# Kernel tuning notes

Measured on AMD Instinct MI355X. Metric: run time of the kernel, lower is better.

Reference implementation:

```python
import jax, jax.numpy as jnp
import numpy as np

D_MODEL = 2048
N_HEADS = 16
D_HEAD = D_MODEL // N_HEADS
EPS = 1e-5


def _layernorm(x, g, b):
    m = jnp.mean(x, axis=-1, keepdims=True)
    v = jnp.mean(jnp.square(x - m), axis=-1, keepdims=True)
    return (x - m) * jax.lax.rsqrt(v + EPS) * g + b


def _mha(x, Wq, bq, Wk, bk, Wv, bv, Wo, bo):
    b, s, _ = x.shape
    # torch Linear: y = x @ W.T + b ; W is [out, in]
    q = (x @ Wq.T + bq).reshape(b, s, N_HEADS, D_HEAD).transpose(0, 2, 1, 3)
    k = (x @ Wk.T + bk).reshape(b, s, N_HEADS, D_HEAD).transpose(0, 2, 1, 3)
    v = (x @ Wv.T + bv).reshape(b, s, N_HEADS, D_HEAD).transpose(0, 2, 1, 3)
    scores = jnp.einsum('bhqd,bhkd->bhqk', q, k) / np.sqrt(D_HEAD).astype(np.float32)
    score = jax.nn.softmax(scores, axis=-1)
    o = jnp.einsum('bhqk,bhkd->bhqd', score, v)
    # NOTE: original does .contiguous().view(b, -1, d_model) WITHOUT transposing
    # heads back -> head-major flattening. Replicated faithfully via reshape.
    o = o.reshape(b, s, D_MODEL)
    return o @ Wo.T + bo, score


def setup_inputs() -> dict:
    key = jax.random.key(0)
    ks = jax.random.split(key, 16)
    sd = 1.0 / np.sqrt(D_MODEL)
    sdf = 1.0 / np.sqrt(4 * D_MODEL)
    d = {
        'x': jax.random.normal(ks[0], (2, 2048, D_MODEL), jnp.float32),
        'Wq': jax.random.uniform(ks[1], (D_MODEL, D_MODEL), jnp.float32, -sd, sd),
        'bq': jnp.zeros((D_MODEL,), jnp.float32),
        'Wk': jax.random.uniform(ks[2], (D_MODEL, D_MODEL), jnp.float32, -sd, sd),
        'bk': jnp.zeros((D_MODEL,), jnp.float32),
        'Wv': jax.random.uniform(ks[3], (D_MODEL, D_MODEL), jnp.float32, -sd, sd),
        'bv': jnp.zeros((D_MODEL,), jnp.float32),
        'Wo': jax.random.uniform(ks[4], (D_MODEL, D_MODEL), jnp.float32, -sd, sd),
        'bo': jnp.zeros((D_MODEL,), jnp.float32),
        'ln1_g': jnp.ones((D_MODEL,), jnp.float32),
        'ln1_b': jnp.zeros((D_MODEL,), jnp.float32),
        'W1': jax.random.uniform(ks[5], (4 * D_MODEL, D_MODEL), jnp.float32, -sd, sd),
        'b1': jnp.zeros((4 * D_MODEL,), jnp.float32),
        'W2': jax.random.uniform(ks[6], (D_MODEL, 4 * D_MODEL), jnp.float32, -sdf, sdf),
        'b2': jnp.zeros((D_MODEL,), jnp.float32),
        'ln2_g': jnp.ones((D_MODEL,), jnp.float32),
        'ln2_b': jnp.zeros((D_MODEL,), jnp.float32),
    }
    return d


def reference(x, Wq, bq, Wk, bk, Wv, bv, Wo, bo, ln1_g, ln1_b, W1, b1, W2, b2, ln2_g, ln2_b):
    # Pre-norm self-attention block (is_post_norm=False, is_cross=False).
    # Dropout is identity (eval mode).
    x_ = _layernorm(x, ln1_g, ln1_b)
    attn_out, score = _mha(x_, Wq, bq, Wk, bk, Wv, bv, Wo, bo)
    x = x + attn_out
    x_ = _layernorm(x, ln2_g, ln2_b)
    h = jax.nn.relu(x_ @ W1.T + b1)
    x = x + (h @ W2.T + b2)
    return x, score
```

## Files before the change

### kernel.cpp

```cpp
#include <hip/hip_runtime.h>
#include <math.h>

#define D_MODEL 2048
#define NHEADS  16
#define DHEAD   128
#define SEQ     2048
#define BATCH   2
#define ROWS    (BATCH * SEQ)
#define D_FF    (4 * D_MODEL)

typedef __attribute__((ext_vector_type(8))) short bf16x8;
typedef __attribute__((ext_vector_type(4))) float f32x4;

__device__ __forceinline__ unsigned short f2bf(float f) {
    unsigned int u = __float_as_uint(f);
    u += 0x7fffu + ((u >> 16) & 1u);
    return (unsigned short)(u >> 16);
}

__device__ __forceinline__ float block_reduce(float v, int is_max) {
    __shared__ float tmp[4];
    #pragma unroll
    for (int o = 32; o > 0; o >>= 1) {
        float other = __shfl_down(v, o, 64);
        v = is_max ? fmaxf(v, other) : (v + other);
    }
    __syncthreads();
    if ((threadIdx.x & 63) == 0) tmp[threadIdx.x >> 6] = v;
    __syncthreads();
    float r = is_max ? fmaxf(fmaxf(tmp[0], tmp[1]), fmaxf(tmp[2], tmp[3]))
                     : (tmp[0] + tmp[1] + tmp[2] + tmp[3]);
    return r;
}

__global__ __launch_bounds__(256)
void castbf_kernel(const float* __restrict__ in, unsigned short* __restrict__ out, int n4)
{
    int i = blockIdx.x * 256 + threadIdx.x;
    if (i < n4) {
        float4 v = ((const float4*)in)[i];
        ushort4 o;
        o.x = f2bf(v.x); o.y = f2bf(v.y); o.z = f2bf(v.z); o.w = f2bf(v.w);
        ((ushort4*)out)[i] = o;
    }
}

__global__ __launch_bounds__(256)
void ln_kernel(const float* __restrict__ x, const float* __restrict__ g,
               const float* __restrict__ b, unsigned short* __restrict__ y)
{
    __shared__ float row[D_MODEL];
    const long r = blockIdx.x;
    const float4* xr = (const float4*)(x + r * D_MODEL);
    float s = 0.f;
    for (int i = threadIdx.x; i < D_MODEL / 4; i += 256) {
        float4 v = xr[i];
        ((float4*)row)[i] = v;
        s += v.x + v.y + v.z + v.w;
    }
    s = block_reduce(s, 0);
    const float mean = s * (1.f / D_MODEL);
    float vs = 0.f;
    for (int i = threadIdx.x; i < D_MODEL / 4; i += 256) {
        float4 v = ((const float4*)row)[i];
        float dx = v.x - mean; vs += dx * dx;
        dx = v.y - mean; vs += dx * dx;
        dx = v.z - mean; vs += dx * dx;
        dx = v.w - mean; vs += dx * dx;
    }
    vs = block_reduce(vs, 0);
    const float inv = rsqrtf(vs * (1.f / D_MODEL) + 1e-5f);
    const float4* g4 = (const float4*)g;
    const float4* b4 = (const float4*)b;
    for (int i = threadIdx.x; i < D_MODEL / 4; i += 256) {
        float4 v = ((const float4*)row)[i];
        float4 gg = g4[i], bb = b4[i];
        ushort4 o;
        o.x = f2bf((v.x - mean) * inv * gg.x + bb.x);
        o.y = f2bf((v.y - mean) * inv * gg.y + bb.y);
        o.z = f2bf((v.z - mean) * inv * gg.z + bb.z);
        o.w = f2bf((v.w - mean) * inv * gg.w + bb.w);
        *(ushort4*)(y + r * D_MODEL + i * 4) = o;
    }
}

__global__ __launch_bounds__(256)
void softmax_kernel(float* __restrict__ sc)
{
    __shared__ float row[SEQ];
    float* p = sc + (long)blockIdx.x * SEQ;
    float m = -1e30f;
    for (int i = threadIdx.x; i < SEQ / 4; i += 256) {
        float4 v = ((const float4*)p)[i];
        ((float4*)row)[i] = v;
        m = fmaxf(m, fmaxf(fmaxf(v.x, v.y), fmaxf(v.z, v.w)));
    }
    m = block_reduce(m, 1);
    float sum = 0.f;
    for (int i = threadIdx.x; i < SEQ; i += 256) {
        float e = expf(row[i] - m);
        row[i] = e;
        sum += e;
    }
    sum = block_reduce(sum, 0);
    const float inv = 1.f / sum;
    for (int i = threadIdx.x; i < SEQ / 4; i += 256) {
        float4 v = ((const float4*)p)[i];
        v.x = row[i * 4 + 0] * inv; v.y = row[i * 4 + 1] * inv;
        v.z = row[i * 4 + 2] * inv; v.w = row[i * 4 + 3] * inv;
        ((float4*)p)[i] = v;
    }
}

constexpr int BK = 64;

__device__ __forceinline__ void stage_tile_f32(const float* g, int ld,
                                               unsigned short* lds, int t)
{
    const int row = t >> 1;
    const int half = t & 1;
    char* lbase = (char*)lds + row * 128;
    const float* gr = g + (size_t)row * ld + half * 32;
    #pragma unroll
    for (int c4 = 0; c4 < 4; ++c4) {
        float4 f0 = *(const float4*)(gr + c4 * 8);
        float4 f1 = *(const float4*)(gr + c4 * 8 + 4);
        bf16x8 v;
        v[0] = (short)f2bf(f0.x); v[1] = (short)f2bf(f0.y);
        v[2] = (short)f2bf(f0.z); v[3] = (short)f2bf(f0.w);
        v[4] = (short)f2bf(f1.x); v[5] = (short)f2bf(f1.y);
        v[6] = (short)f2bf(f1.z); v[7] = (short)f2bf(f1.w);
        const int cs = (half * 4 + c4) ^ (row & 7);
        *(bf16x8*)(lbase + cs * 16) = v;
    }
}

__device__ __forceinline__ void stage_tile_bf(const unsigned short* g, int ld,
                                              unsigned short* lds, int t)
{
    const int row = t >> 1;
    const int half = t & 1;
    char* lbase = (char*)lds + row * 128;
    const unsigned short* gr = g + (size_t)row * ld + half * 32;
    #pragma unroll
    for (int c4 = 0; c4 < 4; ++c4) {
        bf16x8 v = *(const bf16x8*)(gr + c4 * 8);
        const int cs = (half * 4 + c4) ^ (row & 7);
        *(bf16x8*)(lbase + cs * 16) = v;
    }
}

__device__ __forceinline__ void stage_lds(const unsigned short* gbase, int ld,
                                          unsigned short* lds, int wid, int lane)
{
    const int l8 = lane >> 3, c8 = lane & 7;
    #pragma unroll
    for (int i = 0; i < 4; ++i) {
        const int rowb = wid * 32 + i * 8;
        const unsigned short* src = gbase + (size_t)(rowb + l8) * ld + c8 * 8;
        unsigned short* dst = lds + rowb * 64;
        __builtin_amdgcn_global_load_lds(
            (const __attribute__((address_space(1))) unsigned int*)src,
            (__attribute__((address_space(3))) unsigned int*)dst, 16, 0, 0);
    }
}

template<bool AF32, bool OUTBF>
__global__ __launch_bounds__(256)
void gemm_mfma(const void* __restrict__ Av, int lda,
               const unsigned short* __restrict__ B, int ldb,
               const float* __restrict__ bias, int biasM,
               const float* __restrict__ resid,
               void* __restrict__ Cv, int ldc,
               int Kdim, float scale, int relu,
               long sAb, long sAh, long sBb, long sBh, long sCb, long sCh,
               int nh)
{
    __shared__ unsigned short As[128 * BK];
    __shared__ unsigned short Bs[128 * BK];

    const int z  = blockIdx.z;
    const int zb = z / nh, zh = z % nh;
    const long aoff = zb * sAb + zh * sAh;
    const float*          Af = (const float*)Av + (AF32 ? aoff : 0);
    const unsigned short* Ah = (const unsigned short*)Av + (AF32 ? 0 : aoff);
    B += zb * sBb + zh * sBh;
    const long coff = zb * sCb + zh * sCh;
    float*          Cf = (float*)Cv + coff;
    unsigned short* Ch = (unsigned short*)Cv + coff;

    const int bm = blockIdx.y * 128;
    const int bn = blockIdx.x * 128;
    const int t  = threadIdx.x;
    const int lane = t & 63;
    const int wid  = t >> 6;
    const int wr = wid >> 1, wc = wid & 1;
    const int li = lane & 15;
    const int g  = lane >> 4;

    f32x4 acc[4][4];
    #pragma unroll
    for (int i = 0; i < 4; ++i)
        #pragma unroll
        for (int j = 0; j < 4; ++j) acc[i][j] = (f32x4){0.f, 0.f, 0.f, 0.f};

    int aoffs[4], boffs[4];
    #pragma unroll
    for (int m = 0; m < 4; ++m) {
        const int ra = wr * 64 + m * 16 + li;
        const int rb = wc * 64 + m * 16 + li;
        if (AF32) {
            aoffs[m] = ra * 128 + ((g ^ (ra & 7)) << 4);
            boffs[m] = rb * 128 + ((g ^ (rb & 7)) << 4);
        } else {
            aoffs[m] = ra * 128 + (g << 4);
            boffs[m] = rb * 128 + (g << 4);
        }
    }

    for (int k0 = 0; k0 < Kdim; k0 += BK) {
        if (AF32) {
            stage_tile_f32(Af + (size_t)bm * lda + k0, lda, As, t);
            stage_tile_bf (B  + (size_t)bn * ldb + k0, ldb, Bs, t);
        } else {
            stage_lds(Ah + (size_t)bm * lda + k0, lda, As, wid, lane);
            stage_lds(B  + (size_t)bn * ldb + k0, ldb, Bs, wid, lane);
        }
        __syncthreads();
        #pragma unroll
        for (int kk = 0; kk < 2; ++kk) {
            const int kb = kk * 64;
            bf16x8 a[4], b[4];
            #pragma unroll
            for (int m = 0; m < 4; ++m) {
                a[m] = *(const bf16x8*)((const char*)As + (aoffs[m] ^ kb));
                b[m] = *(const bf16x8*)((const char*)Bs + (boffs[m] ^ kb));
            }
            #pragma unroll
            for (int m = 0; m < 4; ++m)
                #pragma unroll
                for (int n = 0; n < 4; ++n)
                    acc[m][n] = __builtin_amdgcn_mfma_f32_16x16x32_bf16(
                                    a[m], b[n], acc[m][n], 0, 0, 0);
        }
        __syncthreads();
    }

    const int g4 = g * 4;
    #pragma unroll
    for (int m = 0; m < 4; ++m) {
        #pragma unroll
        for (int n = 0; n < 4; ++n) {
            const int c = bn + wc * 64 + n * 16 + li;
            #pragma unroll
            for (int r = 0; r < 4; ++r) {
                const long R = bm + wr * 64 + m * 16 + g4 + r;
                float v = acc[m][n][r] * scale;
                if (bias)  v += biasM ? bias[R] : bias[c];
                if (resid) v += resid[R * (long)ldc + c];
                if (relu)  v = fmaxf(v, 0.f);
                if (OUTBF) Ch[R * (long)ldc + c] = f2bf(v);
                else       Cf[R * (long)ldc + c] = v;
            }
        }
    }
}

extern "C" void kernel_launch(void* const* d_in, const int* in_sizes, int n_in,
                              void* d_out, int out_size, void* d_ws, size_t ws_size,
                              hipStream_t stream)
{
    const float* x    = (const float*)d_in[0];
    const float* Wq   = (const float*)d_in[1];
    const float* bq   = (const float*)d_in[2];
    const float* Wk   = (const float*)d_in[3];
    const float* bk   = (const float*)d_in[4];
    const float* Wv   = (const float*)d_in[5];
    const float* bv   = (const float*)d_in[6];
    const float* Wo   = (const float*)d_in[7];
    const float* bo   = (const float*)d_in[8];
    const float* ln1g = (const float*)d_in[9];
    const float* ln1b = (const float*)d_in[10];
    const float* W1   = (const float*)d_in[11];
    const float* b1   = (const float*)d_in[12];
    const float* W2   = (const float*)d_in[13];
    const float* b2   = (const float*)d_in[14];
    const float* ln2g = (const float*)d_in[15];
    const float* ln2b = (const float*)d_in[16];

    const long XN = (long)ROWS * D_MODEL;
    float* out_x     = (float*)d_out;
    float* out_score = out_x + XN;

    char* w = (char*)d_ws;
    unsigned short* Qb   = (unsigned short*)(w);
    unsigned short* Kb   = (unsigned short*)(w + (16u << 20));
    unsigned short* Vtb  = (unsigned short*)(w + (32u << 20));
    unsigned short* xlnb = (unsigned short*)(w + (48u << 20));
    unsigned short* hb   = (unsigned short*)(w + (64u << 20));
    float*          x1   = (float*)         (w + (128u << 20));
    unsigned short* Wqb  = (unsigned short*)(w + (160u << 20));
    unsigned short* Wkb  = (unsigned short*)(w + (168u << 20));
    unsigned short* Wvb  = (unsigned short*)(w + (176u << 20));
    unsigned short* Wob  = (unsigned short*)(w + (184u << 20));
    unsigned short* W1b  = (unsigned short*)(w + (192u << 20));
    unsigned short* W2b  = (unsigned short*)(w + (224u << 20));
    unsigned short* Ohb   = xlnb;
    unsigned short* xln2b = Kb;

    const dim3 blk(256);
    const float one = 1.f;
    const float qk_scale = 0.08838834764831843f;
    const long Z4M = (long)SEQ * D_MODEL;
    const long ZSC = (long)SEQ * SEQ;
    const long ZOH = (long)SEQ * DHEAD;

    const int nW = D_MODEL * D_MODEL / 4, nF = D_FF * D_MODEL / 4;
    hipLaunchKernelGGL(castbf_kernel, dim3(nW / 256), blk, 0, stream, Wq, Wqb, nW);
    hipLaunchKernelGGL(castbf_kernel, dim3(nW / 256), blk, 0, stream, Wk, Wkb, nW);
    hipLaunchKernelGGL(castbf_kernel, dim3(nW / 256), blk, 0, stream, Wv, Wvb, nW);
    hipLaunchKernelGGL(castbf_kernel, dim3(nW / 256), blk, 0, stream, Wo, Wob, nW);
    hipLaunchKernelGGL(castbf_kernel, dim3(nF / 256), blk, 0, stream, W1, W1b, nF);
    hipLaunchKernelGGL(castbf_kernel, dim3(nF / 256), blk, 0, stream, W2, W2b, nF);

    hipLaunchKernelGGL(ln_kernel, dim3(ROWS), blk, 0, stream, x, ln1g, ln1b, xlnb);

    hipLaunchKernelGGL((gemm_mfma<false, true>), dim3(D_MODEL / 128, ROWS / 128, 1), blk, 0, stream,
                       xlnb, D_MODEL, Wqb, D_MODEL, bq, 0, nullptr, Qb, D_MODEL,
                       D_MODEL, one, 0, 0L, 0L, 0L, 0L, 0L, 0L, 1);
    hipLaunchKernelGGL((gemm_mfma<false, true>), dim3(D_MODEL / 128, ROWS / 128, 1), blk, 0, stream,
                       xlnb, D_MODEL, Wkb, D_MODEL, bk, 0, nullptr, Kb, D_MODEL,
                       D_MODEL, one, 0, 0L, 0L, 0L, 0L, 0L, 0L, 1);
    hipLaunchKernelGGL((gemm_mfma<false, true>), dim3(SEQ / 128, D_MODEL / 128, BATCH), blk, 0, stream,
                       Wvb, D_MODEL, xlnb, D_MODEL, bv, 1, nullptr, Vtb, SEQ,
                       D_MODEL, one, 0, 0L, 0L, Z4M, 0L, Z4M, 0L, 1);

    hipLaunchKernelGGL((gemm_mfma<false, false>), dim3(SEQ / 128, SEQ / 128, BATCH * NHEADS), blk, 0, stream,
                       Qb, D_MODEL, Kb, D_MODEL, nullptr, 0, nullptr, out_score, SEQ,
                       DHEAD, qk_scale, 0,
                       Z4M, (long)DHEAD, Z4M, (long)DHEAD, (long)NHEADS * ZSC, ZSC, NHEADS);

    hipLaunchKernelGGL(softmax_kernel, dim3(BATCH * NHEADS * SEQ), blk, 0, stream, out_score);

    hipLaunchKernelGGL((gemm_mfma<true, true>), dim3(DHEAD / 128, SEQ / 128, BATCH * NHEADS), blk, 0, stream,
                       out_score, SEQ, Vtb, SEQ, nullptr, 0, nullptr, Ohb, DHEAD,
                       SEQ, one, 0,
                       (long)NHEADS * ZSC, ZSC, Z4M, (long)DHEAD * SEQ,
                       (long)NHEADS * ZOH, ZOH, NHEADS);

    hipLaunchKernelGGL((gemm_mfma<false, false>), dim3(D_MODEL / 128, ROWS / 128, 1), blk, 0, stream,
                       Ohb, D_MODEL, Wob, D_MODEL, bo, 0, x, x1, D_MODEL,
                       D_MODEL, one, 0, 0L, 0L, 0L, 0L, 0L, 0L, 1);

    hipLaunchKernelGGL(ln_kernel, dim3(ROWS), blk, 0, stream, x1, ln2g, ln2b, xln2b);

    hipLaunchKernelGGL((gemm_mfma<false, true>), dim3(D_FF / 128, ROWS / 128, 1), blk, 0, stream,
                       xln2b, D_MODEL, W1b, D_MODEL, b1, 0, nullptr, hb, D_FF,
                       D_MODEL, one, 1, 0L, 0L, 0L, 0L, 0L, 0L, 1);

    hipLaunchKernelGGL((gemm_mfma<false, false>), dim3(D_MODEL / 128, ROWS / 128, 1), blk, 0, stream,
                       hb, D_FF, W2b, D_FF, b2, 0, x1, out_x, D_MODEL,
                       D_FF, one, 0, 0L, 0L, 0L, 0L, 0L, 0L, 1);
}
```

Before: 2.006 ms.

## Emit bf16 probabilities from softmax and stage GEMM epilogue through LDS

Softmax now also writes a bf16 copy of the probabilities, and it reads the normalized values from LDS instead of re-reading global memory. This lets the PV GEMM take bf16 input through the async global_load_lds path, replacing the fp32 staging path with per-element conversion. Every GEMM epilogue now goes through a swizzled LDS buffer so each thread stores contiguous 32-column row segments with vector stores, replacing scattered scalar stores. The cost is an extra bf16 write of the whole score tensor and extra syncs and LDS traffic in the epilogue.

```diff
diff --git a/kernel.cpp b/kernel.cpp
--- a/kernel.cpp
+++ b/kernel.cpp
@@ -85,10 +85,11 @@
 }
 
 __global__ __launch_bounds__(256)
-void softmax_kernel(float* __restrict__ sc)
+void softmax_kernel(float* __restrict__ sc, unsigned short* __restrict__ pb)
 {
     __shared__ float row[SEQ];
     float* p = sc + (long)blockIdx.x * SEQ;
+    unsigned short* pbf = pb + (long)blockIdx.x * SEQ;
     float m = -1e30f;
     for (int i = threadIdx.x; i < SEQ / 4; i += 256) {
         float4 v = ((const float4*)p)[i];
@@ -105,50 +106,16 @@
     sum = block_reduce(sum, 0);
     const float inv = 1.f / sum;
     for (int i = threadIdx.x; i < SEQ / 4; i += 256) {
-        float4 v = ((const float4*)p)[i];
-        v.x = row[i * 4 + 0] * inv; v.y = row[i * 4 + 1] * inv;
-        v.z = row[i * 4 + 2] * inv; v.w = row[i * 4 + 3] * inv;
+        float4 v = ((const float4*)row)[i];
+        v.x *= inv; v.y *= inv; v.z *= inv; v.w *= inv;
         ((float4*)p)[i] = v;
+        ushort4 o;
+        o.x = f2bf(v.x); o.y = f2bf(v.y); o.z = f2bf(v.z); o.w = f2bf(v.w);
+        ((ushort4*)pbf)[i] = o;
     }
 }
 
 constexpr int BK = 64;
-
-__device__ __forceinline__ void stage_tile_f32(const float* g, int ld,
-                                               unsigned short* lds, int t)
-{
-    const int row = t >> 1;
-    const int half = t & 1;
-    char* lbase = (char*)lds + row * 128;
-    const float* gr = g + (size_t)row * ld + half * 32;
-    #pragma unroll
-    for (int c4 = 0; c4 < 4; ++c4) {
-        float4 f0 = *(const float4*)(gr + c4 * 8);
-        float4 f1 = *(const float4*)(gr + c4 * 8 + 4);
-        bf16x8 v;
-        v[0] = (short)f2bf(f0.x); v[1] = (short)f2bf(f0.y);
-        v[2] = (short)f2bf(f0.z); v[3] = (short)f2bf(f0.w);
-        v[4] = (short)f2bf(f1.x); v[5] = (short)f2bf(f1.y);
-        v[6] = (short)f2bf(f1.z); v[7] = (short)f2bf(f1.w);
-        const int cs = (half * 4 + c4) ^ (row & 7);
-        *(bf16x8*)(lbase + cs * 16) = v;
-    }
-}
-
-__device__ __forceinline__ void stage_tile_bf(const unsigned short* g, int ld,
-                                              unsigned short* lds, int t)
-{
-    const int row = t >> 1;
-    const int half = t & 1;
-    char* lbase = (char*)lds + row * 128;
-    const unsigned short* gr = g + (size_t)row * ld + half * 32;
-    #pragma unroll
-    for (int c4 = 0; c4 < 4; ++c4) {
-        bf16x8 v = *(const bf16x8*)(gr + c4 * 8);
-        const int cs = (half * 4 + c4) ^ (row & 7);
-        *(bf16x8*)(lbase + cs * 16) = v;
-    }
-}
 
 __device__ __forceinline__ void stage_lds(const unsigned short* gbase, int ld,
                                           unsigned short* lds, int wid, int lane)
@@ -165,9 +132,9 @@
     }
 }
 
-template<bool AF32, bool OUTBF>
+template<bool OUTBF>
 __global__ __launch_bounds__(256)
-void gemm_mfma(const void* __restrict__ Av, int lda,
+void gemm_mfma(const unsigned short* __restrict__ A, int lda,
                const unsigned short* __restrict__ B, int ldb,
                const float* __restrict__ bias, int biasM,
                const float* __restrict__ resid,
@@ -176,14 +143,13 @@
                long sAb, long sAh, long sBb, long sBh, long sCb, long sCh,
                int nh)
 {
-    __shared__ unsigned short As[128 * BK];
-    __shared__ unsigned short Bs[128 * BK];
+    __shared__ __align__(16) char smem[32768];
+    unsigned short* As = (unsigned short*)smem;
+    unsigned short* Bs = As + 128 * BK;
 
     const int z  = blockIdx.z;
     const int zb = z / nh, zh = z % nh;
-    const long aoff = zb * sAb + zh * sAh;
-    const float*          Af = (const float*)Av + (AF32 ? aoff : 0);
-    const unsigned short* Ah = (const unsigned short*)Av + (AF32 ? 0 : aoff);
+    A += zb * sAb + zh * sAh;
     B += zb * sBb + zh * sBh;
     const long coff = zb * sCb + zh * sCh;
     float*          Cf = (float*)Cv + coff;
@@ -209,23 +175,13 @@
     for (int m = 0; m < 4; ++m) {
         const int ra = wr * 64 + m * 16 + li;
         const int rb = wc * 64 + m * 16 + li;
-        if (AF32) {
-            aoffs[m] = ra * 128 + ((g ^ (ra & 7)) << 4);
-            boffs[m] = rb * 128 + ((g ^ (rb & 7)) << 4);
-        } else {
-            aoffs[m] = ra * 128 + (g << 4);
-            boffs[m] = rb * 128 + (g << 4);
-        }
+        aoffs[m] = ra * 128 + (g << 4);
+        boffs[m] = rb * 128 + (g << 4);
     }
 
     for (int k0 = 0; k0 < Kdim; k0 += BK) {
-        if (AF32) {
-            stage_tile_f32(Af + (size_t)bm * lda + k0, lda, As, t);
-            stage_tile_bf (B  + (size_t)bn * ldb + k0, ldb, Bs, t);
-        } else {
-            stage_lds(Ah + (size_t)bm * lda + k0, lda, As, wid, lane);
-            stage_lds(B  + (size_t)bn * ldb + k0, ldb, Bs, wid, lane);
-        }
+        stage_lds(A + (size_t)bm * lda + k0, lda, As, wid, lane);
+        stage_lds(B + (size_t)bn * ldb + k0, ldb, Bs, wid, lane);
         __syncthreads();
         #pragma unroll
         for (int kk = 0; kk < 2; ++kk) {
@@ -246,22 +202,78 @@
         __syncthreads();
     }
 
+    float* epi = (float*)smem;
     const int g4 = g * 4;
-    #pragma unroll
-    for (int m = 0; m < 4; ++m) {
-        #pragma unroll
-        for (int n = 0; n < 4; ++n) {
-            const int c = bn + wc * 64 + n * 16 + li;
-            #pragma unroll
-            for (int r = 0; r < 4; ++r) {
-                const long R = bm + wr * 64 + m * 16 + g4 + r;
-                float v = acc[m][n][r] * scale;
-                if (bias)  v += biasM ? bias[R] : bias[c];
-                if (resid) v += resid[R * (long)ldc + c];
-                if (relu)  v = fmaxf(v, 0.f);
-                if (OUTBF) Ch[R * (long)ldc + c] = f2bf(v);
-                else       Cf[R * (long)ldc + c] = v;
-            }
+    const int lrow_r = t >> 2, q = t & 3;
+    #pragma unroll
+    for (int p = 0; p < 2; ++p) {
+        __syncthreads();
+        #pragma unroll
+        for (int mm = 0; mm < 2; ++mm) {
+            const int m = 2 * p + mm;
+            #pragma unroll
+            for (int n = 0; n < 4; ++n) {
+                const int col = wc * 64 + n * 16 + li;
+                #pragma unroll
+                for (int r = 0; r < 4; ++r) {
+                    const int lrow = wr * 32 + mm * 16 + g4 + r;
+                    const int byteoff = lrow * 512 + ((((col >> 2) ^ (lrow & 7)) << 4)) + (col & 3) * 4;
+                    *(float*)((char*)epi + byteoff) = acc[m][n][r];
+                }
+            }
+        }
+        __syncthreads();
+        const long grow = bm + (lrow_r >> 5) * 64 + p * 32 + (lrow_r & 31);
+        const int col0 = bn + q * 32;
+        float v[32];
+        #pragma unroll
+        for (int i = 0; i < 8; ++i) {
+            const int byteoff = lrow_r * 512 + ((((q * 8 + i) ^ (lrow_r & 7)) << 4));
+            *(f32x4*)&v[i * 4] = *(const f32x4*)((const char*)epi + byteoff);
+        }
+        #pragma unroll
+        for (int i = 0; i < 32; ++i) v[i] *= scale;
+        if (bias) {
+            if (biasM) {
+                const float bm_ = bias[grow];
+                #pragma unroll
+                for (int i = 0; i < 32; ++i) v[i] += bm_;
+            } else {
+                #pragma unroll
+                for (int i = 0; i < 8; ++i) {
+                    f32x4 bb = *(const f32x4*)(bias + col0 + i * 4);
+                    v[i * 4 + 0] += bb[0]; v[i * 4 + 1] += bb[1];
+                    v[i * 4 + 2] += bb[2]; v[i * 4 + 3] += bb[3];
+                }
+            }
+        }
+        if (resid) {
+            const float* rr = resid + grow * (long)ldc + col0;
+            #pragma unroll
+            for (int i = 0; i < 8; ++i) {
+                f32x4 r4 = *(const f32x4*)(rr + i * 4);
+                v[i * 4 + 0] += r4[0]; v[i * 4 + 1] += r4[1];
+                v[i * 4 + 2] += r4[2]; v[i * 4 + 3] += r4[3];
+            }
+        }
+        if (relu) {
+            #pragma unroll
+            for (int i = 0; i < 32; ++i) v[i] = fmaxf(v[i], 0.f);
+        }
+        if (OUTBF) {
+            unsigned short* cp = Ch + grow * (long)ldc + col0;
+            #pragma unroll
+            for (int i = 0; i < 4; ++i) {
+                bf16x8 o;
+                #pragma unroll
+                for (int j = 0; j < 8; ++j) o[j] = (short)f2bf(v[i * 8 + j]);
+                *(bf16x8*)(cp + i * 8) = o;
+            }
+        } else {
+            float* cp = Cf + grow * (long)ldc + col0;
+            #pragma unroll
+            for (int i = 0; i < 8; ++i)
+                *(f32x4*)(cp + i * 4) = *(const f32x4*)&v[i * 4];
         }
     }
 }
@@ -305,6 +317,7 @@
     unsigned short* Wob  = (unsigned short*)(w + (184u << 20));
     unsigned short* W1b  = (unsigned short*)(w + (192u << 20));
     unsigned short* W2b  = (unsigned short*)(w + (224u << 20));
+    unsigned short* Pb   = (unsigned short*)(w + (256u << 20));
     unsigned short* Ohb   = xlnb;
     unsigned short* xln2b = Kb;
 
@@ -325,40 +338,40 @@
 
     hipLaunchKernelGGL(ln_kernel, dim3(ROWS), blk, 0, stream, x, ln1g, ln1b, xlnb);
 
-    hipLaunchKernelGGL((gemm_mfma<false, true>), dim3(D_MODEL / 128, ROWS / 128, 1), blk, 0, stream,
+    hipLaunchKernelGGL((gemm_mfma<true>), dim3(D_MODEL / 128, ROWS / 128, 1), blk, 0, stream,
                        xlnb, D_MODEL, Wqb, D_MODEL, bq, 0, nullptr, Qb, D_MODEL,
                        D_MODEL, one, 0, 0L, 0L, 0L, 0L, 0L, 0L, 1);
-    hipLaunchKernelGGL((gemm_mfma<false, true>), dim3(D_MODEL / 128, ROWS / 128, 1), blk, 0, stream,
+    hipLaunchKernelGGL((gemm_mfma<true>), dim3(D_MODEL / 128, ROWS / 128, 1), blk, 0, stream,
                        xlnb, D_MODEL, Wkb, D_MODEL, bk, 0, nullptr, Kb, D_MODEL,
                        D_MODEL, one, 0, 0L, 0L, 0L, 0L, 0L, 0L, 1);
-    hipLaunchKernelGGL((gemm_mfma<false, true>), dim3(SEQ / 128, D_MODEL / 128, BATCH), blk, 0, stream,
+    hipLaunchKernelGGL((gemm_mfma<true>), dim3(SEQ / 128, D_MODEL / 128, BATCH), blk, 0, stream,
                        Wvb, D_MODEL, xlnb, D_MODEL, bv, 1, nullptr, Vtb, SEQ,
                        D_MODEL, one, 0, 0L, 0L, Z4M, 0L, Z4M, 0L, 1);
 
-    hipLaunchKernelGGL((gemm_mfma<false, false>), dim3(SEQ / 128, SEQ / 128, BATCH * NHEADS), blk, 0, stream,
+    hipLaunchKernelGGL((gemm_mfma<false>), dim3(SEQ / 128, SEQ / 128, BATCH * NHEADS), blk, 0, stream,
                        Qb, D_MODEL, Kb, D_MODEL, nullptr, 0, nullptr, out_score, SEQ,
                        DHEAD, qk_scale, 0,
                        Z4M, (long)DHEAD, Z4M, (long)DHEAD, (long)NHEADS * ZSC, ZSC, NHEADS);
 
-    hipLaunchKernelGGL(softmax_kernel, dim3(BATCH * NHEADS * SEQ), blk, 0, stream, out_score);
-
-    hipLaunchKernelGGL((gemm_mfma<true, true>), dim3(DHEAD / 128, SEQ / 128, BATCH * NHEADS), blk, 0, stream,
-                       out_score, SEQ, Vtb, SEQ, nullptr, 0, nullptr, Ohb, DHEAD,
+    hipLaunchKernelGGL(softmax_kernel, dim3(BATCH * NHEADS * SEQ), blk, 0, stream, out_score, Pb);
+
+    hipLaunchKernelGGL((gemm_mfma<true>), dim3(DHEAD / 128, SEQ / 128, BATCH * NHEADS), blk, 0, stream,
+                       Pb, SEQ, Vtb, SEQ, nullptr, 0, nullptr, Ohb, DHEAD,
                        SEQ, one, 0,
                        (long)NHEADS * ZSC, ZSC, Z4M, (long)DHEAD * SEQ,
                        (long)NHEADS * ZOH, ZOH, NHEADS);
 
-    hipLaunchKernelGGL((gemm_mfma<false, false>), dim3(D_MODEL / 128, ROWS / 128, 1), blk, 0, stream,
+    hipLaunchKernelGGL((gemm_mfma<false>), dim3(D_MODEL / 128, ROWS / 128, 1), blk, 0, stream,
                        Ohb, D_MODEL, Wob, D_MODEL, bo, 0, x, x1, D_MODEL,
                        D_MODEL, one, 0, 0L, 0L, 0L, 0L, 0L, 0L, 1);
 
     hipLaunchKernelGGL(ln_kernel, dim3(ROWS), blk, 0, stream, x1, ln2g, ln2b, xln2b);
 
-    hipLaunchKernelGGL((gemm_mfma<false, true>), dim3(D_FF / 128, ROWS / 128, 1), blk, 0, stream,
+    hipLaunchKernelGGL((gemm_mfma<true>), dim3(D_FF / 128, ROWS / 128, 1), blk, 0, stream,
                        xln2b, D_MODEL, W1b, D_MODEL, b1, 0, nullptr, hb, D_FF,
                        D_MODEL, one, 1, 0L, 0L, 0L, 0L, 0L, 0L, 1);
 
-    hipLaunchKernelGGL((gemm_mfma<false, false>), dim3(D_MODEL / 128, ROWS / 128, 1), blk, 0, stream,
+    hipLaunchKernelGGL((gemm_mfma<false>), dim3(D_MODEL / 128, ROWS / 128, 1), blk, 0, stream,
                        hb, D_FF, W2b, D_FF, b2, 0, x1, out_x, D_MODEL,
                        D_FF, one, 0, 0L, 0L, 0L, 0L, 0L, 0L, 1);
 }
```

New measurement: 1.969 ms. No clear change (-1.8%).
